# Performance work log

Hardware: AMD Instinct MI355X
Metric: run time of the kernel (lower is better)

The kernel has to match this reference:

```python
import jax, jax.numpy as jnp
import numpy as np

E = 512    # embedding_size
H = 1024   # rnn_hidden_size
C = 20     # num_classes
B = 64     # batch
T = 512    # seq len


def setup_inputs() -> dict:
    key = jax.random.key(0)
    ks = jax.random.split(key, 9)
    s_e = 1.0 / np.sqrt(H)  # torch RNNCell/Linear init scale (uniform bound)
    return {
        "x_in": jax.random.normal(ks[0], (B, T, E), dtype=jnp.float32),
        "W_ih": jax.random.uniform(ks[1], (H, E), jnp.float32, -s_e, s_e),
        "W_hh": jax.random.uniform(ks[2], (H, H), jnp.float32, -s_e, s_e),
        "b_ih": jax.random.uniform(ks[3], (H,), jnp.float32, -s_e, s_e),
        "b_hh": jax.random.uniform(ks[4], (H,), jnp.float32, -s_e, s_e),
        "fc1_w": jax.random.uniform(ks[5], (H, H), jnp.float32, -s_e, s_e),
        "fc1_b": jax.random.uniform(ks[6], (H,), jnp.float32, -s_e, s_e),
        "fc2_w": jax.random.uniform(ks[7], (C, H), jnp.float32, -s_e, s_e),
        "fc2_b": jax.random.uniform(ks[8], (C,), jnp.float32, -s_e, s_e),
    }


def reference(x_in, W_ih, W_hh, b_ih, b_hh, fc1_w, fc1_b, fc2_w, fc2_b):
    # batch_first: [B, T, E] -> [T, B, E]
    x_tbf = jnp.transpose(x_in, (1, 0, 2))
    # Pre-project inputs for all timesteps in one big GEMM: [T, B, H]
    x_proj = jnp.einsum("tbe,he->tbh", x_tbf, W_ih) + b_ih + b_hh

    def step(h, xp_t):
        h_new = jnp.tanh(xp_t + h @ W_hh.T)
        return h_new, None

    h0 = jnp.zeros((x_in.shape[0], W_hh.shape[0]), dtype=x_in.dtype)
    h_last, _ = jax.lax.scan(step, h0, x_proj)

    # MLP head (dropout is identity in eval mode)
    y = jax.nn.relu(h_last @ fc1_w.T + fc1_b)
    y = y @ fc2_w.T + fc2_b
    return y
```

## Files before the change

kernel.cpp:

```cpp
#include <hip/hip_runtime.h>

#define B_ 64
#define T_ 512
#define E_ 512
#define H_ 1024
#define C_ 20
#define RING 16
#define BH (B_ * H_)

typedef __attribute__((ext_vector_type(8))) _Float16 f16x8;
typedef __attribute__((ext_vector_type(4))) float f32x4;
typedef __attribute__((ext_vector_type(4))) unsigned int u32x4;
typedef unsigned long long u64;

__device__ __forceinline__ void st_agent_u64(u64* p, u64 v){
  __hip_atomic_store(p, v, __ATOMIC_RELAXED, __HIP_MEMORY_SCOPE_AGENT);
}
__device__ __forceinline__ u32x4 ld_b128_cohere(const void* p){
  u32x4 r;
  asm volatile("global_load_dwordx4 %0, %1, off sc0 sc1"
               : "=v"(r) : "v"(p) : "memory");
  return r;
}

__global__ void prep_kernel(const float* __restrict__ wih,
                            const float* __restrict__ whh,
                            _Float16* __restrict__ whhF,
                            _Float16* __restrict__ wihF,
                            short* __restrict__ hring)
{
  const long NH = (long)H_ * H_;
  const long NI = (long)H_ * E_;
  const long NR = (long)RING * BH;
  const long TOT = NH + NI + NR;
  long i = (long)blockIdx.x * blockDim.x + threadIdx.x;
  const long stride = (long)gridDim.x * blockDim.x;
  for (; i < TOT; i += stride){
    if (i < NH){
      whhF[i] = (_Float16)whh[i];
    } else if (i < NH + NI){
      long j = i - NH;
      wihF[j] = (_Float16)wih[j];
    } else {
      long j = i - NH - NI;
      hring[j] = (j < BH) ? (short)0 : (short)0xFFFF;
    }
  }
}

__global__ __launch_bounds__(256, 1) void xp_gemm(
    const float* __restrict__ x, const _Float16* __restrict__ wihF,
    const float* __restrict__ bih, const float* __restrict__ bhh,
    _Float16* __restrict__ xp)
{
  const int lane = threadIdx.x & 63;
  const int wv   = threadIdx.x >> 6;
  const int bg   = blockIdx.x & 3;
  const int tb   = (blockIdx.x >> 2) * 4;
  const int r16  = lane & 15;
  const int k8   = (lane >> 4) * 8;

  const int brow = bg * 16 + r16;

  f32x4 acc[4][16];
  #pragma unroll
  for (int t = 0; t < 4; t++)
    #pragma unroll
    for (int c = 0; c < 16; c++) acc[t][c] = { 0.f, 0.f, 0.f, 0.f };

  for (int kc = 0; kc < 16; kc++){
    f16x8 a[4];
    #pragma unroll
    for (int t = 0; t < 4; t++){
      const float* xp8 = x + ((long)brow * T_ + tb + t) * E_ + kc * 32 + k8;
      float4 f0 = *(const float4*)xp8;
      float4 f1 = *(const float4*)(xp8 + 4);
      f16x8 v;
      v[0]=(_Float16)f0.x; v[1]=(_Float16)f0.y; v[2]=(_Float16)f0.z; v[3]=(_Float16)f0.w;
      v[4]=(_Float16)f1.x; v[5]=(_Float16)f1.y; v[6]=(_Float16)f1.z; v[7]=(_Float16)f1.w;
      a[t] = v;
    }
    #pragma unroll
    for (int c = 0; c < 16; c++){
      f16x8 b = *(const f16x8*)(wihF + (long)(wv * 256 + c * 16 + r16) * E_ + kc * 32 + k8);
      #pragma unroll
      for (int t = 0; t < 4; t++)
        acc[t][c] = __builtin_amdgcn_mfma_f32_16x16x32_f16(a[t], b, acc[t][c], 0, 0, 0);
    }
  }
  #pragma unroll
  for (int c = 0; c < 16; c++){
    int col = wv * 256 + c * 16 + r16;
    float bs = bih[col] + bhh[col];
    #pragma unroll
    for (int t = 0; t < 4; t++){
      #pragma unroll
      for (int j = 0; j < 4; j++){
        int row = bg * 16 + (lane >> 4) * 4 + j;
        xp[((long)(tb + t)) * BH + (long)row * H_ + col] =
            (_Float16)(acc[t][c][j] + bs);
      }
    }
  }
}

__global__ __launch_bounds__(512, 1) void rnn_scan(
    const _Float16* __restrict__ xp, const _Float16* __restrict__ whhF,
    _Float16* __restrict__ hring, float* __restrict__ hT)
{
  const int tid  = threadIdx.x;
  const int lane = tid & 63;
  const int w    = tid >> 6;
  const int bg   = blockIdx.x & 3;
  const int cg   = blockIdx.x >> 2;
  const int r16  = lane & 15;
  const int kq   = lane >> 4;

  __shared__ float part[8][16][132];

  f16x8 wh[8][4];
  #pragma unroll
  for (int ct = 0; ct < 8; ct++)
    #pragma unroll
    for (int kc = 0; kc < 4; kc++)
      wh[ct][kc] = *(const f16x8*)(whhF +
          (long)(cg * 128 + ct * 16 + r16) * H_ + w * 128 + kc * 32 + kq * 8);
  #pragma unroll
  for (int ct = 0; ct < 8; ct++)
    #pragma unroll
    for (int kc = 0; kc < 4; kc++)
      asm volatile("" : "+v"(wh[ct][kc]));

  const long haOff = (long)(bg * 16 + r16) * H_ + w * 128 + kq * 8;
  const int  rr  = tid >> 5;
  const int  cc4 = tid & 31;
  const long pubOff = (long)(bg * 16 + rr) * H_ + cg * 128 + cc4 * 4;

  union { _Float16 h[4]; u64 q; } xc, xn;
  xc.q = *(const u64*)(xp + pubOff);
  xn.q = 0;

  for (int t = 0; t < T_; ++t){
    const _Float16* hb = hring + (long)(t & (RING - 1)) * BH + haOff;
    u32x4 q[4];
    #pragma unroll
    for (int c = 0; c < 4; c++) q[c] = ld_b128_cohere(hb + c * 32);
    asm volatile("s_waitcnt vmcnt(0)" ::: "memory");
    __builtin_amdgcn_sched_barrier(0);

    f32x4 acc[8];
    #pragma unroll
    for (int ct = 0; ct < 8; ct++) acc[ct] = { 0.f, 0.f, 0.f, 0.f };

    unsigned need = 0xFu;
    while (true){
      #pragma unroll
      for (int c = 0; c < 4; c++){
        if (need & (1u << c)){
          bool bad = ((q[c][0] & 0xFFFFu) == 0xFFFFu) ||
                     ((q[c][2] & 0xFFFFu) == 0xFFFFu);
          if (!__any(bad)){
            union { u32x4 u; f16x8 v; } hu; hu.u = q[c];
            #pragma unroll
            for (int ct = 0; ct < 8; ct++)
              acc[ct] = __builtin_amdgcn_mfma_f32_16x16x32_f16(hu.v, wh[ct][c], acc[ct], 0, 0, 0);
            need &= ~(1u << c);
          }
        }
      }
      if (!need) break;
      #pragma unroll
      for (int c = 0; c < 4; c++)
        if (need & (1u << c)) q[c] = ld_b128_cohere(hb + c * 32);
      asm volatile("s_waitcnt vmcnt(0)" ::: "memory");
      __builtin_amdgcn_sched_barrier(0);
    }

    if (t + 1 < T_)
      xn.q = *(const u64*)(xp + (long)(t + 1) * BH + pubOff);

    #pragma unroll
    for (int ct = 0; ct < 8; ct++)
      #pragma unroll
      for (int j = 0; j < 4; j++)
        part[w][kq * 4 + j][ct * 16 + r16] = acc[ct][j];
    asm volatile("s_waitcnt lgkmcnt(0)\n\ts_barrier" ::: "memory");

    {
      f32x4 s = *(const f32x4*)&part[0][rr][cc4 * 4];
      #pragma unroll
      for (int p = 1; p < 8; p++)
        s += *(const f32x4*)&part[p][rr][cc4 * 4];
      float hv[4];
      #pragma unroll
      for (int j = 0; j < 4; j++){
        float v = s[j] + (float)xc.h[j];
        float a = fabsf(v), ex = __expf(-2.f * a);
        hv[j] = copysignf((1.f - ex) / (1.f + ex), v);
      }

      if (t < T_ - 1){
        union { _Float16 h[4]; u64 q; } g;
        #pragma unroll
        for (int j = 0; j < 4; j++) g.h[j] = (_Float16)hv[j];
        st_agent_u64((u64*)(hring + (long)((t + 1) & (RING - 1)) * BH + pubOff), g.q);
        if (t + 8 < T_)
          st_agent_u64((u64*)(hring + (long)((t + 8) & (RING - 1)) * BH + pubOff),
                       0xFFFFFFFFFFFFFFFFull);
      } else {
        *(float4*)(hT + pubOff) = make_float4(hv[0], hv[1], hv[2], hv[3]);
      }
    }
    asm volatile("s_waitcnt lgkmcnt(0)\n\ts_barrier" ::: "memory");
    xc.q = xn.q;
  }
}

__global__ void fc1_kernel(const float* __restrict__ hT, const float* __restrict__ w1,
                           const float* __restrict__ b1, float* __restrict__ y1)
{
  int o = blockIdx.x * 256 + threadIdx.x;
  int b = o >> 10, j = o & 1023;
  const float4* hp = (const float4*)(hT + (long)b * H_);
  const float4* wp = (const float4*)(w1 + (long)j * H_);
  float s = 0.f;
  #pragma unroll 4
  for (int k = 0; k < H_ / 4; k++){
    float4 hv = hp[k], wv = wp[k];
    s += hv.x * wv.x + hv.y * wv.y + hv.z * wv.z + hv.w * wv.w;
  }
  s += b1[j];
  y1[o] = s > 0.f ? s : 0.f;
}

__global__ void fc2_kernel(const float* __restrict__ y1, const float* __restrict__ w2,
                           const float* __restrict__ b2, float* __restrict__ out)
{
  __shared__ float ybuf[H_];
  int b = blockIdx.x;
  for (int k = threadIdx.x; k < H_; k += 256) ybuf[k] = y1[(long)b * H_ + k];
  __syncthreads();
  if (threadIdx.x < C_){
    const float* wp = w2 + (long)threadIdx.x * H_;
    float s = 0.f;
    for (int k = 0; k < H_; k++) s += ybuf[k] * wp[k];
    out[b * C_ + threadIdx.x] = s + b2[threadIdx.x];
  }
}

extern "C" void kernel_launch(void* const* d_in, const int* in_sizes, int n_in,
                              void* d_out, int out_size, void* d_ws, size_t ws_size,
                              hipStream_t stream)
{
  const float* x   = (const float*)d_in[0];
  const float* wih = (const float*)d_in[1];
  const float* whh = (const float*)d_in[2];
  const float* bih = (const float*)d_in[3];
  const float* bhh = (const float*)d_in[4];
  const float* w1  = (const float*)d_in[5];
  const float* b1  = (const float*)d_in[6];
  const float* w2  = (const float*)d_in[7];
  const float* b2  = (const float*)d_in[8];
  float* out = (float*)d_out;

  char* ws = (char*)d_ws;
  size_t off = 0;
  auto carve = [&](size_t bytes) -> char* {
    char* p = ws + off; off += (bytes + 255) & ~(size_t)255; return p;
  };
  _Float16* whhF  = (_Float16*)carve((size_t)H_ * H_ * 2);
  _Float16* wihF  = (_Float16*)carve((size_t)H_ * E_ * 2);
  _Float16* hring = (_Float16*)carve((size_t)RING * BH * 2);
  float*    hT    = (float*)carve((size_t)B_ * H_ * 4);
  float*    y1    = (float*)carve((size_t)B_ * H_ * 4);
  _Float16* xp    = (_Float16*)carve((size_t)T_ * BH * 2);

  prep_kernel<<<1024, 256, 0, stream>>>(wih, whh, whhF, wihF, (short*)hring);
  xp_gemm<<<512, 256, 0, stream>>>(x, wihF, bih, bhh, xp);
  rnn_scan<<<32, 512, 0, stream>>>(xp, whhF, hring, hT);
  fc1_kernel<<<256, 256, 0, stream>>>(hT, w1, b1, y1);
  fc2_kernel<<<64, 256, 0, stream>>>(y1, w2, b2, out);
}
```

Baseline: 1.576 ms.

## Fuse input projection into recurrent scan and double-buffer the reduction LDS

Removes the separate xp_gemm kernel and its fp16 xp buffer. Each scan block now keeps its slice of W_ih in registers and computes the next timestep's input projection with MFMAs while waiting on the step barrier; the result seeds the recurrent accumulator and the bias is added during the reduction. The partial-sum LDS is double-buffered so one of the two per-step barriers can be dropped. The cost is more register pressure and extra MFMA and global load work on the latency-critical serial path, in exchange for no xp memory traffic and one fewer kernel launch.

Result: slower. 3.524 ms (+123.6%).

```diff
diff --git a/kernel.cpp b/kernel.cpp
--- a/kernel.cpp
+++ b/kernel.cpp
@@ -48,64 +48,10 @@
   }
 }
 
-__global__ __launch_bounds__(256, 1) void xp_gemm(
+__global__ __launch_bounds__(512, 1) void rnn_scan(
     const float* __restrict__ x, const _Float16* __restrict__ wihF,
+    const _Float16* __restrict__ whhF,
     const float* __restrict__ bih, const float* __restrict__ bhh,
-    _Float16* __restrict__ xp)
-{
-  const int lane = threadIdx.x & 63;
-  const int wv   = threadIdx.x >> 6;
-  const int bg   = blockIdx.x & 3;
-  const int tb   = (blockIdx.x >> 2) * 4;
-  const int r16  = lane & 15;
-  const int k8   = (lane >> 4) * 8;
-
-  const int brow = bg * 16 + r16;
-
-  f32x4 acc[4][16];
-  #pragma unroll
-  for (int t = 0; t < 4; t++)
-    #pragma unroll
-    for (int c = 0; c < 16; c++) acc[t][c] = { 0.f, 0.f, 0.f, 0.f };
-
-  for (int kc = 0; kc < 16; kc++){
-    f16x8 a[4];
-    #pragma unroll
-    for (int t = 0; t < 4; t++){
-      const float* xp8 = x + ((long)brow * T_ + tb + t) * E_ + kc * 32 + k8;
-      float4 f0 = *(const float4*)xp8;
-      float4 f1 = *(const float4*)(xp8 + 4);
-      f16x8 v;
-      v[0]=(_Float16)f0.x; v[1]=(_Float16)f0.y; v[2]=(_Float16)f0.z; v[3]=(_Float16)f0.w;
-      v[4]=(_Float16)f1.x; v[5]=(_Float16)f1.y; v[6]=(_Float16)f1.z; v[7]=(_Float16)f1.w;
-      a[t] = v;
-    }
-    #pragma unroll
-    for (int c = 0; c < 16; c++){
-      f16x8 b = *(const f16x8*)(wihF + (long)(wv * 256 + c * 16 + r16) * E_ + kc * 32 + k8);
-      #pragma unroll
-      for (int t = 0; t < 4; t++)
-        acc[t][c] = __builtin_amdgcn_mfma_f32_16x16x32_f16(a[t], b, acc[t][c], 0, 0, 0);
-    }
-  }
-  #pragma unroll
-  for (int c = 0; c < 16; c++){
-    int col = wv * 256 + c * 16 + r16;
-    float bs = bih[col] + bhh[col];
-    #pragma unroll
-    for (int t = 0; t < 4; t++){
-      #pragma unroll
-      for (int j = 0; j < 4; j++){
-        int row = bg * 16 + (lane >> 4) * 4 + j;
-        xp[((long)(tb + t)) * BH + (long)row * H_ + col] =
-            (_Float16)(acc[t][c][j] + bs);
-      }
-    }
-  }
-}
-
-__global__ __launch_bounds__(512, 1) void rnn_scan(
-    const _Float16* __restrict__ xp, const _Float16* __restrict__ whhF,
     _Float16* __restrict__ hring, float* __restrict__ hT)
 {
   const int tid  = threadIdx.x;
@@ -115,8 +61,9 @@
   const int cg   = blockIdx.x >> 2;
   const int r16  = lane & 15;
   const int kq   = lane >> 4;
-
-  __shared__ float part[8][16][132];
+  const int k8   = kq * 8;
+
+  __shared__ float part[2][8][16][132];
 
   f16x8 wh[8][4];
   #pragma unroll
@@ -124,21 +71,57 @@
     #pragma unroll
     for (int kc = 0; kc < 4; kc++)
       wh[ct][kc] = *(const f16x8*)(whhF +
-          (long)(cg * 128 + ct * 16 + r16) * H_ + w * 128 + kc * 32 + kq * 8);
+          (long)(cg * 128 + ct * 16 + r16) * H_ + w * 128 + kc * 32 + k8);
+  f16x8 wi[8][2];
   #pragma unroll
   for (int ct = 0; ct < 8; ct++)
     #pragma unroll
-    for (int kc = 0; kc < 4; kc++)
-      asm volatile("" : "+v"(wh[ct][kc]));
-
-  const long haOff = (long)(bg * 16 + r16) * H_ + w * 128 + kq * 8;
+    for (int ec = 0; ec < 2; ec++)
+      wi[ct][ec] = *(const f16x8*)(wihF +
+          (long)(cg * 128 + ct * 16 + r16) * E_ + w * 64 + ec * 32 + k8);
+  #pragma unroll
+  for (int ct = 0; ct < 8; ct++){
+    #pragma unroll
+    for (int kc = 0; kc < 4; kc++) asm volatile("" : "+v"(wh[ct][kc]));
+    asm volatile("" : "+v"(wi[ct][0]), "+v"(wi[ct][1]));
+  }
+
+  const long haOff = (long)(bg * 16 + r16) * H_ + w * 128 + k8;
   const int  rr  = tid >> 5;
   const int  cc4 = tid & 31;
   const long pubOff = (long)(bg * 16 + rr) * H_ + cg * 128 + cc4 * 4;
 
-  union { _Float16 h[4]; u64 q; } xc, xn;
-  xc.q = *(const u64*)(xp + pubOff);
-  xn.q = 0;
+  f32x4 bias4;
+  #pragma unroll
+  for (int j = 0; j < 4; j++){
+    int col = cg * 128 + cc4 * 4 + j;
+    bias4[j] = bih[col] + bhh[col];
+  }
+
+  auto load_xa = [&](int tn, int ec) -> f16x8 {
+    const float* xp8 = x + ((long)(bg * 16 + r16) * T_ + tn) * E_
+                         + w * 64 + ec * 32 + k8;
+    float4 f0 = *(const float4*)xp8;
+    float4 f1 = *(const float4*)(xp8 + 4);
+    f16x8 v;
+    v[0]=(_Float16)f0.x; v[1]=(_Float16)f0.y; v[2]=(_Float16)f0.z; v[3]=(_Float16)f0.w;
+    v[4]=(_Float16)f1.x; v[5]=(_Float16)f1.y; v[6]=(_Float16)f1.z; v[7]=(_Float16)f1.w;
+    return v;
+  };
+
+  f32x4 xpacc[8];
+  {
+    f16x8 xa0 = load_xa(0, 0), xa1 = load_xa(0, 1);
+    #pragma unroll
+    for (int ct = 0; ct < 8; ct++){
+      f32x4 z = { 0.f, 0.f, 0.f, 0.f };
+      z = __builtin_amdgcn_mfma_f32_16x16x32_f16(xa0, wi[ct][0], z, 0, 0, 0);
+      z = __builtin_amdgcn_mfma_f32_16x16x32_f16(xa1, wi[ct][1], z, 0, 0, 0);
+      xpacc[ct] = z;
+    }
+  }
+  f16x8 xa_cur[2], xa_nxt[2];
+  xa_cur[0] = load_xa(1, 0); xa_cur[1] = load_xa(1, 1);
 
   for (int t = 0; t < T_; ++t){
     const _Float16* hb = hring + (long)(t & (RING - 1)) * BH + haOff;
@@ -150,7 +133,7 @@
 
     f32x4 acc[8];
     #pragma unroll
-    for (int ct = 0; ct < 8; ct++) acc[ct] = { 0.f, 0.f, 0.f, 0.f };
+    for (int ct = 0; ct < 8; ct++) acc[ct] = xpacc[ct];
 
     unsigned need = 0xFu;
     while (true){
@@ -176,25 +159,41 @@
       __builtin_amdgcn_sched_barrier(0);
     }
 
-    if (t + 1 < T_)
-      xn.q = *(const u64*)(xp + (long)(t + 1) * BH + pubOff);
-
-    #pragma unroll
-    for (int ct = 0; ct < 8; ct++)
-      #pragma unroll
-      for (int j = 0; j < 4; j++)
-        part[w][kq * 4 + j][ct * 16 + r16] = acc[ct][j];
+    {
+      float (*buf)[16][132] = part[t & 1];
+      #pragma unroll
+      for (int ct = 0; ct < 8; ct++)
+        #pragma unroll
+        for (int j = 0; j < 4; j++)
+          buf[w][kq * 4 + j][ct * 16 + r16] = acc[ct][j];
+    }
+
+    if (t + 1 < T_){
+      #pragma unroll
+      for (int ct = 0; ct < 8; ct++){
+        f32x4 z = { 0.f, 0.f, 0.f, 0.f };
+        z = __builtin_amdgcn_mfma_f32_16x16x32_f16(xa_cur[0], wi[ct][0], z, 0, 0, 0);
+        z = __builtin_amdgcn_mfma_f32_16x16x32_f16(xa_cur[1], wi[ct][1], z, 0, 0, 0);
+        xpacc[ct] = z;
+      }
+      if (t + 2 < T_){
+        xa_nxt[0] = load_xa(t + 2, 0);
+        xa_nxt[1] = load_xa(t + 2, 1);
+      }
+    }
+
     asm volatile("s_waitcnt lgkmcnt(0)\n\ts_barrier" ::: "memory");
 
     {
-      f32x4 s = *(const f32x4*)&part[0][rr][cc4 * 4];
-      #pragma unroll
-      for (int p = 1; p < 8; p++)
-        s += *(const f32x4*)&part[p][rr][cc4 * 4];
+      const float (*buf)[16][132] = part[t & 1];
+      f32x4 s = bias4;
+      #pragma unroll
+      for (int p = 0; p < 8; p++)
+        s += *(const f32x4*)&buf[p][rr][cc4 * 4];
       float hv[4];
       #pragma unroll
       for (int j = 0; j < 4; j++){
-        float v = s[j] + (float)xc.h[j];
+        float v = s[j];
         float a = fabsf(v), ex = __expf(-2.f * a);
         hv[j] = copysignf((1.f - ex) / (1.f + ex), v);
       }
@@ -211,8 +210,8 @@
         *(float4*)(hT + pubOff) = make_float4(hv[0], hv[1], hv[2], hv[3]);
       }
     }
-    asm volatile("s_waitcnt lgkmcnt(0)\n\ts_barrier" ::: "memory");
-    xc.q = xn.q;
+
+    xa_cur[0] = xa_nxt[0]; xa_cur[1] = xa_nxt[1];
   }
 }
 
@@ -273,11 +272,9 @@
   _Float16* hring = (_Float16*)carve((size_t)RING * BH * 2);
   float*    hT    = (float*)carve((size_t)B_ * H_ * 4);
   float*    y1    = (float*)carve((size_t)B_ * H_ * 4);
-  _Float16* xp    = (_Float16*)carve((size_t)T_ * BH * 2);
 
   prep_kernel<<<1024, 256, 0, stream>>>(wih, whh, whhF, wihF, (short*)hring);
-  xp_gemm<<<512, 256, 0, stream>>>(x, wihF, bih, bhh, xp);
-  rnn_scan<<<32, 512, 0, stream>>>(xp, whhF, hring, hT);
+  rnn_scan<<<32, 512, 0, stream>>>(x, wihF, whhF, bih, bhh, hring, hT);
   fc1_kernel<<<256, 256, 0, stream>>>(hT, w1, b1, y1);
   fc2_kernel<<<64, 256, 0, stream>>>(y1, w2, b2, out);
 }
```
